# Kernel tuning notes

Hardware: AMD Instinct MI355X
Metric: run time of the kernel (lower is better)

The kernel has to match this reference:

```python
import jax, jax.numpy as jnp
import numpy as np

N = 100000
E = 1600000
H = 4
C = 128
F_IN = 182
D = H * C  # 512
NEG_SLOPE = 0.2
LN_EPS = 1e-5


def _p(key, shape, scale=0.05):
    return jax.random.normal(key, shape, dtype=jnp.float32) * scale


def setup_inputs() -> dict:
    key = jax.random.key(0)
    ks = jax.random.split(key, 20)
    x = jax.random.normal(ks[0], (N, F_IN), dtype=jnp.float32)
    edge_index = jax.random.randint(ks[1], (2, E), 0, N, dtype=jnp.int64)
    inp = {
        "x": x,
        "edge_index": edge_index,
        # GAT layer 1
        "W1": _p(ks[2], (F_IN, D)),
        "a_src1": _p(ks[3], (H, C)),
        "a_dst1": _p(ks[4], (H, C)),
        "b1": _p(ks[5], (D,)),
        "g1": jnp.ones((D,), jnp.float32),
        "be1": jnp.zeros((D,), jnp.float32),
        # GAT layer 2
        "W2": _p(ks[6], (D, D)),
        "a_src2": _p(ks[7], (H, C)),
        "a_dst2": _p(ks[8], (H, C)),
        "b2": _p(ks[9], (D,)),
        "g2": jnp.ones((D,), jnp.float32),
        "be2": jnp.zeros((D,), jnp.float32),
        # classifier MLP
        "Wc1": _p(ks[10], (D, D)),
        "bc1": jnp.zeros((D,), jnp.float32),
        "Wc2": _p(ks[11], (D, 2)),
        "bc2": jnp.zeros((2,), jnp.float32),
    }
    return inp


def _gat_conv(x, src, dst, W, a_src, a_dst, b):
    # x: [N, Fin] -> h: [N, H, C]
    h = (x @ W).reshape(N, H, C)
    # per-node attention contributions: [N, H]
    s_src = jnp.sum(h * a_src, axis=-1)
    s_dst = jnp.sum(h * a_dst, axis=-1)
    # per-edge raw score: [E+N, H]
    e = jax.nn.leaky_relu(s_src[src] + s_dst[dst], NEG_SLOPE)
    # segment softmax over incoming edges of each dst node
    emax = jax.ops.segment_max(e, dst, num_segments=N)
    p = jnp.exp(e - emax[dst])
    denom = jax.ops.segment_sum(p, dst, num_segments=N)
    alpha = p / denom[dst]  # [E+N, H]
    # weighted aggregation of source features: [N, H, C]
    out = jax.ops.segment_sum(alpha[:, :, None] * h[src], dst, num_segments=N)
    return out.reshape(N, D) + b


def _layer_norm(x, g, b):
    mu = jnp.mean(x, axis=-1, keepdims=True)
    var = jnp.mean(jnp.square(x - mu), axis=-1, keepdims=True)
    return (x - mu) * jax.lax.rsqrt(var + LN_EPS) * g + b


def reference(x, edge_index, W1, a_src1, a_dst1, b1, g1, be1,
              W2, a_src2, a_dst2, b2, g2, be2, Wc1, bc1, Wc2, bc2):
    # add self-loops (PyG GATConv default)
    loops = jnp.arange(N, dtype=edge_index.dtype)
    src = jnp.concatenate([edge_index[0], loops])
    dst = jnp.concatenate([edge_index[1], loops])

    h1 = _gat_conv(x, src, dst, W1, a_src1, a_dst1, b1)
    h1 = jax.nn.elu(_layer_norm(h1, g1, be1))
    h2 = _gat_conv(h1, src, dst, W2, a_src2, a_dst2, b2)
    h2 = jax.nn.elu(_layer_norm(h2, g2, be2))
    # classifier (dropout is identity in eval)
    z = jax.nn.relu(h2 @ Wc1 + bc1)
    return z @ Wc2 + bc2
```

## Files before the change

### kernel.cpp

```cpp
#include <hip/hip_runtime.h>
#include <math.h>

static constexpr int N_NODES = 100000;
static constexpr int N_EDGES = 1600000;
static constexpr int E_TOT   = N_NODES + N_EDGES;
static constexpr int D   = 512;
static constexpr int FIN = 182;
static constexpr int K1P = 192;
static constexpr int M_PAD = 100096;
static constexpr float NEG_SLOPE = 0.2f;
static constexpr float LN_EPS = 1e-5f;

typedef __attribute__((ext_vector_type(8))) short short8;
typedef __attribute__((ext_vector_type(4))) float floatx4;

__device__ __forceinline__ unsigned short f2bf(float f) {
  unsigned int x = __builtin_bit_cast(unsigned int, f);
  x += 0x7fffu + ((x >> 16) & 1u);
  return (unsigned short)(x >> 16);
}
__device__ __forceinline__ void unpack2(unsigned int w, float& lo, float& hi) {
  lo = __builtin_bit_cast(float, w << 16);
  hi = __builtin_bit_cast(float, w & 0xffff0000u);
}

typedef __attribute__((address_space(1))) const void gv_t;
typedef __attribute__((address_space(3))) void lv_t;
__device__ __forceinline__ void gll16(const void* g, void* l) {
  __builtin_amdgcn_global_load_lds((gv_t*)g, (lv_t*)l, 16, 0, 0);
}

__global__ __launch_bounds__(256) void k_init(int* __restrict__ deg,
                                              int* __restrict__ counter,
                                              int* __restrict__ flag) {
  int i = blockIdx.x * 256 + threadIdx.x;
  if (i < N_NODES) deg[i] = 0;
  if (i == 0) { *counter = 0; *flag = 0; }
}

__global__ __launch_bounds__(256) void k_detect(const int* __restrict__ ei,
                                                int* __restrict__ flag) {
  bool nz = false;
#pragma unroll
  for (int r = 0; r < 8; ++r) {
    int i = threadIdx.x + r * 256;
    nz |= (ei[2 * i + 1] != 0);
  }
  __shared__ int sh[4];
  int wv = threadIdx.x >> 6;
  if ((threadIdx.x & 63) == 0) sh[wv] = 0;
  __syncthreads();
  if (__any(nz) && (threadIdx.x & 63) == 0) sh[wv] = 1;
  __syncthreads();
  if (threadIdx.x == 0) *flag = sh[0] | sh[1] | sh[2] | sh[3];
}

__device__ __forceinline__ int edge_src(const int* ei, int f, int i) {
  return f ? ei[i] : ei[2 * i];
}
__device__ __forceinline__ int edge_dst(const int* ei, int f, int i) {
  return f ? ei[N_EDGES + i] : ei[2 * (N_EDGES + i)];
}

__global__ __launch_bounds__(256) void k_count(const int* __restrict__ ei,
                                               const int* __restrict__ flag,
                                               int* __restrict__ deg) {
  int i = blockIdx.x * 256 + threadIdx.x;
  if (i >= E_TOT) return;
  int f = *flag;
  int d = (i < N_EDGES) ? edge_dst(ei, f, i) : (i - N_EDGES);
  atomicAdd(deg + d, 1);
}

__global__ __launch_bounds__(256) void k_alloc(const int* __restrict__ deg,
                                               int* __restrict__ off,
                                               int* __restrict__ pos,
                                               int* __restrict__ counter) {
  int i = blockIdx.x * 256 + threadIdx.x;
  if (i >= N_NODES) return;
  int r = atomicAdd(counter, deg[i]);
  off[i] = r;
  pos[i] = r;
}

__global__ __launch_bounds__(256) void k_fill(const int* __restrict__ ei,
                                              const int* __restrict__ flag,
                                              int* __restrict__ pos,
                                              int* __restrict__ csr_src) {
  int i = blockIdx.x * 256 + threadIdx.x;
  if (i >= E_TOT) return;
  int f = *flag;
  int s, d;
  if (i < N_EDGES) { s = edge_src(ei, f, i); d = edge_dst(ei, f, i); }
  else             { s = d = i - N_EDGES; }
  int slot = atomicAdd(pos + d, 1);
  csr_src[slot] = s;
}

__global__ __launch_bounds__(256) void k_cvt_x(const float* __restrict__ x,
                                               unsigned short* __restrict__ xb) {
  int i = blockIdx.x * 256 + threadIdx.x;
  if (i >= N_NODES * K1P) return;
  int row = i / K1P, col = i - row * K1P;
  float v = (col < FIN) ? x[(size_t)row * FIN + col] : 0.f;
  xb[i] = f2bf(v);
}

__global__ __launch_bounds__(256) void k_cvt_wt(const float* __restrict__ W,
                                                unsigned short* __restrict__ Wt,
                                                int K, int Kpad) {
  int i = blockIdx.x * 256 + threadIdx.x;
  if (i >= 512 * Kpad) return;
  int n = i / Kpad, k = i - n * Kpad;
  Wt[i] = f2bf(k < K ? W[(size_t)k * 512 + n] : 0.f);
}

__global__ __launch_bounds__(256) void k_out_init(const float* __restrict__ bc2,
                                                  float* __restrict__ out) {
  int i = blockIdx.x * 256 + threadIdx.x;
  if (i < N_NODES) {
    float2 v; v.x = bc2[0]; v.y = bc2[1];
    ((float2*)out)[i] = v;
  }
}

__global__ __launch_bounds__(256)
void gemm_mfma(const unsigned short* __restrict__ A,
               const unsigned short* __restrict__ Bt,
               unsigned short* __restrict__ C,
               int lda)
{
  __shared__ unsigned short As[128 * 32];
  __shared__ unsigned short Bs[128 * 32];
  const int t    = threadIdx.x;
  const int w    = t >> 6;
  const int lane = t & 63;
  const int r    = lane & 15;
  const int q    = lane >> 4;
  const int bm   = blockIdx.y * 128;
  const int bn   = blockIdx.x * 128;
  const int wm   = (w >> 1) * 64;
  const int wn   = (w & 1) * 64;

  const int ch0 = (w * 2 + 0) * 64 + lane;
  const int ch1 = (w * 2 + 1) * 64 + lane;
  const unsigned short* gA0 = A + (size_t)(bm + (ch0 >> 2)) * lda + (ch0 & 3) * 8;
  const unsigned short* gA1 = A + (size_t)(bm + (ch1 >> 2)) * lda + (ch1 & 3) * 8;
  const unsigned short* gB0 = Bt + (size_t)(bn + (ch0 >> 2)) * lda + (ch0 & 3) * 8;
  const unsigned short* gB1 = Bt + (size_t)(bn + (ch1 >> 2)) * lda + (ch1 & 3) * 8;
  unsigned short* lA0 = As + (w * 2 + 0) * 512;
  unsigned short* lA1 = As + (w * 2 + 1) * 512;
  unsigned short* lB0 = Bs + (w * 2 + 0) * 512;
  unsigned short* lB1 = Bs + (w * 2 + 1) * 512;

  floatx4 acc[4][4] = {};

  for (int k0 = 0; k0 < lda; k0 += 32) {
    gll16(gA0 + k0, lA0);
    gll16(gA1 + k0, lA1);
    gll16(gB0 + k0, lB0);
    gll16(gB1 + k0, lB1);
    __syncthreads();

    short8 af[4], bfr[4];
#pragma unroll
    for (int im = 0; im < 4; ++im)
      af[im] = *(const short8*)(As + (wm + im * 16 + r) * 32 + q * 8);
#pragma unroll
    for (int in = 0; in < 4; ++in)
      bfr[in] = *(const short8*)(Bs + (wn + in * 16 + r) * 32 + q * 8);
#pragma unroll
    for (int im = 0; im < 4; ++im)
#pragma unroll
      for (int in = 0; in < 4; ++in)
        acc[im][in] = __builtin_amdgcn_mfma_f32_16x16x32_bf16(
            af[im], bfr[in], acc[im][in], 0, 0, 0);
    __syncthreads();
  }

#pragma unroll
  for (int in = 0; in < 4; ++in) {
    const int col = bn + wn + in * 16 + r;
#pragma unroll
    for (int im = 0; im < 4; ++im) {
      const size_t rowbase = (size_t)(bm + wm + im * 16 + q * 4) * 512 + col;
#pragma unroll
      for (int rr = 0; rr < 4; ++rr)
        C[rowbase + (size_t)rr * 512] = f2bf(acc[im][in][rr]);
    }
  }
}

__global__ __launch_bounds__(256)
void gemm_cls(const unsigned short* __restrict__ A,
              const unsigned short* __restrict__ Bt,
              const float* __restrict__ bc1,
              const float* __restrict__ Wc2,
              float* __restrict__ out,
              int lda)
{
  __shared__ unsigned short As[128 * 32];
  __shared__ unsigned short Bs[128 * 32];
  const int t    = threadIdx.x;
  const int w    = t >> 6;
  const int lane = t & 63;
  const int r    = lane & 15;
  const int q    = lane >> 4;
  const int bm   = blockIdx.y * 128;
  const int bn   = blockIdx.x * 128;
  const int wm   = (w >> 1) * 64;
  const int wn   = (w & 1) * 64;

  const int ch0 = (w * 2 + 0) * 64 + lane;
  const int ch1 = (w * 2 + 1) * 64 + lane;
  const unsigned short* gA0 = A + (size_t)(bm + (ch0 >> 2)) * lda + (ch0 & 3) * 8;
  const unsigned short* gA1 = A + (size_t)(bm + (ch1 >> 2)) * lda + (ch1 & 3) * 8;
  const unsigned short* gB0 = Bt + (size_t)(bn + (ch0 >> 2)) * lda + (ch0 & 3) * 8;
  const unsigned short* gB1 = Bt + (size_t)(bn + (ch1 >> 2)) * lda + (ch1 & 3) * 8;
  unsigned short* lA0 = As + (w * 2 + 0) * 512;
  unsigned short* lA1 = As + (w * 2 + 1) * 512;
  unsigned short* lB0 = Bs + (w * 2 + 0) * 512;
  unsigned short* lB1 = Bs + (w * 2 + 1) * 512;

  floatx4 acc[4][4] = {};

  for (int k0 = 0; k0 < lda; k0 += 32) {
    gll16(gA0 + k0, lA0);
    gll16(gA1 + k0, lA1);
    gll16(gB0 + k0, lB0);
    gll16(gB1 + k0, lB1);
    __syncthreads();

    short8 af[4], bfr[4];
#pragma unroll
    for (int im = 0; im < 4; ++im)
      af[im] = *(const short8*)(As + (wm + im * 16 + r) * 32 + q * 8);
#pragma unroll
    for (int in = 0; in < 4; ++in)
      bfr[in] = *(const short8*)(Bs + (wn + in * 16 + r) * 32 + q * 8);
#pragma unroll
    for (int im = 0; im < 4; ++im)
#pragma unroll
      for (int in = 0; in < 4; ++in)
        acc[im][in] = __builtin_amdgcn_mfma_f32_16x16x32_bf16(
            af[im], bfr[in], acc[im][in], 0, 0, 0);
    __syncthreads();
  }

  float p0[16], p1[16];
#pragma unroll
  for (int k = 0; k < 16; ++k) { p0[k] = 0.f; p1[k] = 0.f; }

#pragma unroll
  for (int in = 0; in < 4; ++in) {
    const int col = bn + wn + in * 16 + r;
    const float bv = bc1[col];
    const float w0 = Wc2[col * 2 + 0];
    const float w1 = Wc2[col * 2 + 1];
#pragma unroll
    for (int im = 0; im < 4; ++im)
#pragma unroll
      for (int rr = 0; rr < 4; ++rr) {
        float z = fmaxf(acc[im][in][rr] + bv, 0.f);
        p0[im * 4 + rr] += z * w0;
        p1[im * 4 + rr] += z * w1;
      }
  }
#pragma unroll
  for (int o2 = 1; o2 < 16; o2 <<= 1) {
#pragma unroll
    for (int k = 0; k < 16; ++k) {
      p0[k] += __shfl_xor(p0[k], o2);
      p1[k] += __shfl_xor(p1[k], o2);
    }
  }
  if (r == 0) {
#pragma unroll
    for (int im = 0; im < 4; ++im)
#pragma unroll
      for (int rr = 0; rr < 4; ++rr) {
        int row = bm + wm + im * 16 + q * 4 + rr;
        if (row < N_NODES) {
          atomicAdd(out + (size_t)row * 2,     p0[im * 4 + rr]);
          atomicAdd(out + (size_t)row * 2 + 1, p1[im * 4 + rr]);
        }
      }
  }
}

__global__ __launch_bounds__(256) void k_sdots(const unsigned short* __restrict__ h,
                                               const float* __restrict__ a_src,
                                               const float* __restrict__ a_dst,
                                               float2* __restrict__ ssc,
                                               float* __restrict__ s_dst,
                                               unsigned char* __restrict__ h8) {
  int node = blockIdx.x * 4 + (threadIdx.x >> 6);
  int lane = threadIdx.x & 63;
  if (node >= N_NODES) return;
  uint4 w = ((const uint4*)(h + (size_t)node * D))[lane];
  float v[8];
  unpack2(w.x, v[0], v[1]); unpack2(w.y, v[2], v[3]);
  unpack2(w.z, v[4], v[5]); unpack2(w.w, v[6], v[7]);

  float am = 0.f;
#pragma unroll
  for (int k = 0; k < 8; ++k) am = fmaxf(am, fabsf(v[k]));
#pragma unroll
  for (int o = 1; o < 16; o <<= 1) am = fmaxf(am, __shfl_xor(am, o));
  am = fmaxf(am, 1e-20f);
  const float qsc = 127.f / am;
  int qv[8];
#pragma unroll
  for (int k = 0; k < 8; ++k) qv[k] = (int)rintf(v[k] * qsc) + 128;
  uint2 pk;
  pk.x = (qv[0] & 255) | ((qv[1] & 255) << 8) | ((qv[2] & 255) << 16) | ((qv[3] & 255) << 24);
  pk.y = (qv[4] & 255) | ((qv[5] & 255) << 8) | ((qv[6] & 255) << 16) | ((qv[7] & 255) << 24);
  ((uint2*)(h8 + (size_t)node * 512))[lane] = pk;

  const float4* as = (const float4*)a_src;
  const float4* ad = (const float4*)a_dst;
  float4 s0 = as[lane*2], s1 = as[lane*2+1];
  float4 d0 = ad[lane*2], d1 = ad[lane*2+1];
  float ps = v[0]*s0.x + v[1]*s0.y + v[2]*s0.z + v[3]*s0.w
           + v[4]*s1.x + v[5]*s1.y + v[6]*s1.z + v[7]*s1.w;
  float pd = v[0]*d0.x + v[1]*d0.y + v[2]*d0.z + v[3]*d0.w
           + v[4]*d1.x + v[5]*d1.y + v[6]*d1.z + v[7]*d1.w;
#pragma unroll
  for (int o = 1; o < 16; o <<= 1) {
    ps += __shfl_xor(ps, o);
    pd += __shfl_xor(pd, o);
  }
  if ((lane & 15) == 0) {
    int hh = lane >> 4;
    float2 sc; sc.x = ps; sc.y = am * (1.f / 127.f);
    ssc[node*4 + hh] = sc;
    s_dst[node*4 + hh] = pd;
  }
}

__global__ __launch_bounds__(256) void k_aggregate(const unsigned char* __restrict__ h8,
                                                   const float2* __restrict__ ssc,
                                                   const int* __restrict__ csr_src,
                                                   const int* __restrict__ off,
                                                   const int* __restrict__ deg,
                                                   const float* __restrict__ s_dst,
                                                   const float* __restrict__ bvec,
                                                   const float* __restrict__ gvec,
                                                   const float* __restrict__ bevec,
                                                   unsigned short* __restrict__ out) {
  int node = blockIdx.x * 4 + (threadIdx.x >> 6);
  int lane = threadIdx.x & 63;
  if (node >= N_NODES) return;
  const int o   = __builtin_amdgcn_readfirstlane(off[node]);
  const int cnt = __builtin_amdgcn_readfirstlane(deg[node]);
  const int head = lane >> 4;
  const float sdH = s_dst[(size_t)node * 4 + head];

  float acc[8] = {0.f,0.f,0.f,0.f,0.f,0.f,0.f,0.f};
  float sum = 0.f, sum_ps = 0.f;

  int s_cur = __builtin_amdgcn_readfirstlane(csr_src[o]);
  uint2 w_cur = ((const uint2*)(h8 + (size_t)s_cur * 512))[lane];
  float2 fc_cur = ssc[(size_t)s_cur * 4 + head];

  for (int j = 0; j < cnt; ++j) {
    int jn = (j + 1 < cnt) ? (j + 1) : j;
    int s_nxt = __builtin_amdgcn_readfirstlane(csr_src[o + jn]);
    uint2 w_nxt = ((const uint2*)(h8 + (size_t)s_nxt * 512))[lane];
    float2 fc_nxt = ssc[(size_t)s_nxt * 4 + head];

    float e = fc_cur.x + sdH;
    e = (e > 0.f) ? e : NEG_SLOPE * e;
    float p = __expf(e);
    sum += p;
    float ps = p * fc_cur.y;
    sum_ps += ps;
    unsigned int wx = w_cur.x, wy = w_cur.y;
    acc[0] += ps * (float)( wx        & 255u);
    acc[1] += ps * (float)((wx >>  8) & 255u);
    acc[2] += ps * (float)((wx >> 16) & 255u);
    acc[3] += ps * (float)( wx >> 24);
    acc[4] += ps * (float)( wy        & 255u);
    acc[5] += ps * (float)((wy >>  8) & 255u);
    acc[6] += ps * (float)((wy >> 16) & 255u);
    acc[7] += ps * (float)( wy >> 24);

    s_cur = s_nxt; w_cur = w_nxt; fc_cur = fc_nxt;
  }

  const float inv = 1.f / sum;
  const float4* bb = (const float4*)bvec;
  float4 b0 = bb[lane*2], b1 = bb[lane*2+1];
  float bl[8] = {b0.x,b0.y,b0.z,b0.w,b1.x,b1.y,b1.z,b1.w};
#pragma unroll
  for (int k = 0; k < 8; ++k)
    acc[k] = (acc[k] - 128.f * sum_ps) * inv + bl[k];

  float ps2 = 0.f, pq = 0.f;
#pragma unroll
  for (int k = 0; k < 8; ++k) { ps2 += acc[k]; pq += acc[k]*acc[k]; }
#pragma unroll
  for (int o2 = 1; o2 < 64; o2 <<= 1) {
    ps2 += __shfl_xor(ps2, o2);
    pq  += __shfl_xor(pq, o2);
  }
  float mu  = ps2 * (1.f/512.f);
  float var = pq * (1.f/512.f) - mu*mu;
  float rstd = rsqrtf(var + LN_EPS);

  const float4* gg = (const float4*)gvec;
  const float4* ee = (const float4*)bevec;
  float4 g0 = gg[lane*2], g1 = gg[lane*2+1];
  float4 e0 = ee[lane*2], e1 = ee[lane*2+1];
  float gs[8] = {g0.x,g0.y,g0.z,g0.w,g1.x,g1.y,g1.z,g1.w};
  float es[8] = {e0.x,e0.y,e0.z,e0.w,e1.x,e1.y,e1.z,e1.w};

  unsigned short us[8];
#pragma unroll
  for (int k = 0; k < 8; ++k) {
    float y = (acc[k] - mu) * rstd * gs[k] + es[k];
    y = (y > 0.f) ? y : expm1f(y);
    us[k] = f2bf(y);
  }
  uint4 w;
  w.x = (unsigned int)us[0] | ((unsigned int)us[1] << 16);
  w.y = (unsigned int)us[2] | ((unsigned int)us[3] << 16);
  w.z = (unsigned int)us[4] | ((unsigned int)us[5] << 16);
  w.w = (unsigned int)us[6] | ((unsigned int)us[7] << 16);
  ((uint4*)(out + (size_t)node * D))[lane] = w;
}

extern "C" void kernel_launch(void* const* d_in, const int* in_sizes, int n_in,
                              void* d_out, int out_size, void* d_ws, size_t ws_size,
                              hipStream_t stream) {
  const float* x      = (const float*)d_in[0];
  const int*   ei     = (const int*)  d_in[1];
  const float* W1     = (const float*)d_in[2];
  const float* a_src1 = (const float*)d_in[3];
  const float* a_dst1 = (const float*)d_in[4];
  const float* b1     = (const float*)d_in[5];
  const float* g1     = (const float*)d_in[6];
  const float* be1    = (const float*)d_in[7];
  const float* W2     = (const float*)d_in[8];
  const float* a_src2 = (const float*)d_in[9];
  const float* a_dst2 = (const float*)d_in[10];
  const float* b2     = (const float*)d_in[11];
  const float* g2     = (const float*)d_in[12];
  const float* be2    = (const float*)d_in[13];
  const float* Wc1    = (const float*)d_in[14];
  const float* bc1    = (const float*)d_in[15];
  const float* Wc2    = (const float*)d_in[16];
  const float* bc2    = (const float*)d_in[17];
  float* outp = (float*)d_out;

  char* p = (char*)d_ws;
  auto alloc = [&](size_t bytes) {
    char* r = p;
    p += (bytes + 255) & ~(size_t)255;
    return r;
  };
  unsigned short* hbuf = (unsigned short*)alloc((size_t)M_PAD * D * 2);
  unsigned short* obuf = (unsigned short*)alloc((size_t)M_PAD * D * 2);
  unsigned short* w1t  = (unsigned short*)alloc((size_t)512 * K1P * 2);
  unsigned short* w2t  = (unsigned short*)alloc((size_t)512 * 512 * 2);
  unsigned short* wc1t = (unsigned short*)alloc((size_t)512 * 512 * 2);
  int*   csr_src = (int*)  alloc((size_t)E_TOT * 4);
  int*   deg     = (int*)  alloc((size_t)N_NODES * 4);
  int*   off     = (int*)  alloc((size_t)N_NODES * 4);
  int*   pos     = (int*)  alloc((size_t)N_NODES * 4);
  int*   counter = (int*)  alloc(256);
  int*   flag    = (int*)  alloc(256);
  float2* ssc    = (float2*)alloc((size_t)N_NODES * 4 * 8);
  float* s_dst   = (float*)alloc((size_t)N_NODES * 4 * 4);
  unsigned char* h8 = (unsigned char*)alloc((size_t)M_PAD * 512);
  unsigned short* xb = obuf;

  const int EB = (E_TOT + 255) / 256;
  const int NB = (N_NODES + 255) / 256;
  const int NW = (N_NODES + 3) / 4;
  dim3 gg(4, M_PAD / 128);

  k_init  <<<NB, 256, 0, stream>>>(deg, counter, flag);
  k_detect<<<1, 256, 0, stream>>>(ei, flag);
  k_count <<<EB, 256, 0, stream>>>(ei, flag, deg);
  k_alloc <<<NB, 256, 0, stream>>>(deg, off, pos, counter);
  k_fill  <<<EB, 256, 0, stream>>>(ei, flag, pos, csr_src);

  k_cvt_x <<<(N_NODES * K1P + 255) / 256, 256, 0, stream>>>(x, xb);
  k_cvt_wt<<<(512 * K1P + 255) / 256, 256, 0, stream>>>(W1, w1t, FIN, K1P);
  k_cvt_wt<<<(512 * 512 + 255) / 256, 256, 0, stream>>>(W2, w2t, 512, 512);
  k_cvt_wt<<<(512 * 512 + 255) / 256, 256, 0, stream>>>(Wc1, wc1t, 512, 512);
  k_out_init<<<NB, 256, 0, stream>>>(bc2, outp);

  gemm_mfma  <<<gg, 256, 0, stream>>>(xb, w1t, hbuf, K1P);
  k_sdots    <<<NW, 256, 0, stream>>>(hbuf, a_src1, a_dst1, ssc, s_dst, h8);
  k_aggregate<<<NW, 256, 0, stream>>>(h8, ssc, csr_src, off, deg,
                                      s_dst, b1, g1, be1, obuf);

  gemm_mfma  <<<gg, 256, 0, stream>>>(obuf, w2t, hbuf, 512);
  k_sdots    <<<NW, 256, 0, stream>>>(hbuf, a_src2, a_dst2, ssc, s_dst, h8);
  k_aggregate<<<NW, 256, 0, stream>>>(h8, ssc, csr_src, off, deg,
                                      s_dst, b2, g2, be2, obuf);

  gemm_cls   <<<gg, 256, 0, stream>>>(obuf, wc1t, bc1, Wc2, outp, 512);
}
```

Before: 1.012 ms.

## Fuse attention dots and int8 quantization into GEMM epilogue, merge detect into init

The per-node attention score dot products, per-head absmax and int8 quantization now run in the MFMA GEMM epilogue, using cross-lane shuffles and LDS reductions. This removes the bf16 h buffer write, its re-read by the separate k_sdots kernel, and one launch per layer. The h8 layout changes to a column interleave that follows the MFMA lane mapping, so the aggregate kernel now loads bias, gamma and beta and writes its output with a matching permuted index pattern. The edge-format detection is folded into k_init's first block to drop one more launch.

```diff
diff --git a/kernel.cpp b/kernel.cpp
--- a/kernel.cpp
+++ b/kernel.cpp
@@ -30,29 +30,30 @@
   __builtin_amdgcn_global_load_lds((gv_t*)g, (lv_t*)l, 16, 0, 0);
 }
 
-__global__ __launch_bounds__(256) void k_init(int* __restrict__ deg,
+__global__ __launch_bounds__(256) void k_init(const int* __restrict__ ei,
+                                              int* __restrict__ deg,
                                               int* __restrict__ counter,
                                               int* __restrict__ flag) {
   int i = blockIdx.x * 256 + threadIdx.x;
   if (i < N_NODES) deg[i] = 0;
-  if (i == 0) { *counter = 0; *flag = 0; }
-}
-
-__global__ __launch_bounds__(256) void k_detect(const int* __restrict__ ei,
-                                                int* __restrict__ flag) {
-  bool nz = false;
-#pragma unroll
-  for (int r = 0; r < 8; ++r) {
-    int i = threadIdx.x + r * 256;
-    nz |= (ei[2 * i + 1] != 0);
-  }
-  __shared__ int sh[4];
-  int wv = threadIdx.x >> 6;
-  if ((threadIdx.x & 63) == 0) sh[wv] = 0;
-  __syncthreads();
-  if (__any(nz) && (threadIdx.x & 63) == 0) sh[wv] = 1;
-  __syncthreads();
-  if (threadIdx.x == 0) *flag = sh[0] | sh[1] | sh[2] | sh[3];
+  if (blockIdx.x == 0) {
+    bool nz = false;
+#pragma unroll
+    for (int rp = 0; rp < 8; ++rp) {
+      int j = threadIdx.x + rp * 256;
+      nz |= (ei[2 * j + 1] != 0);
+    }
+    __shared__ int sh[4];
+    int wv = threadIdx.x >> 6;
+    if ((threadIdx.x & 63) == 0) sh[wv] = 0;
+    __syncthreads();
+    if (__any(nz) && (threadIdx.x & 63) == 0) sh[wv] = 1;
+    __syncthreads();
+    if (threadIdx.x == 0) {
+      *flag = sh[0] | sh[1] | sh[2] | sh[3];
+      *counter = 0;
+    }
+  }
 }
 
 __device__ __forceinline__ int edge_src(const int* ei, int f, int i) {
@@ -125,10 +126,14 @@
 }
 
 __global__ __launch_bounds__(256)
-void gemm_mfma(const unsigned short* __restrict__ A,
-               const unsigned short* __restrict__ Bt,
-               unsigned short* __restrict__ C,
-               int lda)
+void gemm_fused(const unsigned short* __restrict__ A,
+                const unsigned short* __restrict__ Bt,
+                const float* __restrict__ a_src,
+                const float* __restrict__ a_dst,
+                float2* __restrict__ ssc,
+                float* __restrict__ s_dst,
+                unsigned char* __restrict__ h8,
+                int lda)
 {
   __shared__ unsigned short As[128 * 32];
   __shared__ unsigned short Bs[128 * 32];
@@ -178,15 +183,82 @@
     __syncthreads();
   }
 
+  float* sred = (float*)As;
+  float* qscl = (float*)Bs;
+
+  float asv[4], adv[4];
 #pragma unroll
   for (int in = 0; in < 4; ++in) {
-    const int col = bn + wn + in * 16 + r;
-#pragma unroll
-    for (int im = 0; im < 4; ++im) {
-      const size_t rowbase = (size_t)(bm + wm + im * 16 + q * 4) * 512 + col;
-#pragma unroll
-      for (int rr = 0; rr < 4; ++rr)
-        C[rowbase + (size_t)rr * 512] = f2bf(acc[im][in][rr]);
+    asv[in] = a_src[bn + wn + in * 16 + r];
+    adv[in] = a_dst[bn + wn + in * 16 + r];
+  }
+#pragma unroll
+  for (int im = 0; im < 4; ++im) {
+    float ps_[4], pd_[4], pm_[4];
+#pragma unroll
+    for (int rr = 0; rr < 4; ++rr) {
+      float s = 0.f, d = 0.f, m = 0.f;
+#pragma unroll
+      for (int in = 0; in < 4; ++in) {
+        float v = acc[im][in][rr];
+        s += v * asv[in];
+        d += v * adv[in];
+        m = fmaxf(m, fabsf(v));
+      }
+      ps_[rr] = s; pd_[rr] = d; pm_[rr] = m;
+    }
+#pragma unroll
+    for (int o2 = 1; o2 < 16; o2 <<= 1) {
+#pragma unroll
+      for (int rr = 0; rr < 4; ++rr) {
+        ps_[rr] += __shfl_xor(ps_[rr], o2);
+        pd_[rr] += __shfl_xor(pd_[rr], o2);
+        pm_[rr] = fmaxf(pm_[rr], __shfl_xor(pm_[rr], o2));
+      }
+    }
+    if (r == 0) {
+#pragma unroll
+      for (int rr = 0; rr < 4; ++rr) {
+        int r64 = im * 16 + q * 4 + rr;
+        sred[(w * 64 + r64) * 4 + 0] = ps_[rr];
+        sred[(w * 64 + r64) * 4 + 1] = pd_[rr];
+        sred[(w * 64 + r64) * 4 + 2] = pm_[rr];
+      }
+    }
+  }
+  __syncthreads();
+
+  if (t < 128) {
+    int hf = t >> 6;
+    int r64 = t & 63;
+    const float* pa = sred + ((hf * 2 + 0) * 64 + r64) * 4;
+    const float* pb = sred + ((hf * 2 + 1) * 64 + r64) * 4;
+    float s  = pa[0] + pb[0];
+    float dd = pa[1] + pb[1];
+    float am = fmaxf(fmaxf(pa[2], pb[2]), 1e-20f);
+    qscl[t] = 127.f / am;
+    int node = bm + t;
+    if (node < N_NODES) {
+      float2 sc; sc.x = s; sc.y = am * (1.f / 127.f);
+      ssc[(size_t)node * 4 + blockIdx.x] = sc;
+      s_dst[(size_t)node * 4 + blockIdx.x] = dd;
+    }
+  }
+  __syncthreads();
+
+#pragma unroll
+  for (int im = 0; im < 4; ++im) {
+#pragma unroll
+    for (int rr = 0; rr < 4; ++rr) {
+      int lr = wm + im * 16 + q * 4 + rr;
+      float qs = qscl[lr];
+      unsigned int pk = 0;
+#pragma unroll
+      for (int in = 0; in < 4; ++in) {
+        int qv = (int)rintf(acc[im][in][rr] * qs) + 128;
+        pk |= (unsigned int)(qv & 255) << (8 * in);
+      }
+      *(unsigned int*)(h8 + (size_t)(bm + lr) * 512 + bn + wn + 4 * r) = pk;
     }
   }
 }
@@ -288,56 +360,6 @@
   }
 }
 
-__global__ __launch_bounds__(256) void k_sdots(const unsigned short* __restrict__ h,
-                                               const float* __restrict__ a_src,
-                                               const float* __restrict__ a_dst,
-                                               float2* __restrict__ ssc,
-                                               float* __restrict__ s_dst,
-                                               unsigned char* __restrict__ h8) {
-  int node = blockIdx.x * 4 + (threadIdx.x >> 6);
-  int lane = threadIdx.x & 63;
-  if (node >= N_NODES) return;
-  uint4 w = ((const uint4*)(h + (size_t)node * D))[lane];
-  float v[8];
-  unpack2(w.x, v[0], v[1]); unpack2(w.y, v[2], v[3]);
-  unpack2(w.z, v[4], v[5]); unpack2(w.w, v[6], v[7]);
-
-  float am = 0.f;
-#pragma unroll
-  for (int k = 0; k < 8; ++k) am = fmaxf(am, fabsf(v[k]));
-#pragma unroll
-  for (int o = 1; o < 16; o <<= 1) am = fmaxf(am, __shfl_xor(am, o));
-  am = fmaxf(am, 1e-20f);
-  const float qsc = 127.f / am;
-  int qv[8];
-#pragma unroll
-  for (int k = 0; k < 8; ++k) qv[k] = (int)rintf(v[k] * qsc) + 128;
-  uint2 pk;
-  pk.x = (qv[0] & 255) | ((qv[1] & 255) << 8) | ((qv[2] & 255) << 16) | ((qv[3] & 255) << 24);
-  pk.y = (qv[4] & 255) | ((qv[5] & 255) << 8) | ((qv[6] & 255) << 16) | ((qv[7] & 255) << 24);
-  ((uint2*)(h8 + (size_t)node * 512))[lane] = pk;
-
-  const float4* as = (const float4*)a_src;
-  const float4* ad = (const float4*)a_dst;
-  float4 s0 = as[lane*2], s1 = as[lane*2+1];
-  float4 d0 = ad[lane*2], d1 = ad[lane*2+1];
-  float ps = v[0]*s0.x + v[1]*s0.y + v[2]*s0.z + v[3]*s0.w
-           + v[4]*s1.x + v[5]*s1.y + v[6]*s1.z + v[7]*s1.w;
-  float pd = v[0]*d0.x + v[1]*d0.y + v[2]*d0.z + v[3]*d0.w
-           + v[4]*d1.x + v[5]*d1.y + v[6]*d1.z + v[7]*d1.w;
-#pragma unroll
-  for (int o = 1; o < 16; o <<= 1) {
-    ps += __shfl_xor(ps, o);
-    pd += __shfl_xor(pd, o);
-  }
-  if ((lane & 15) == 0) {
-    int hh = lane >> 4;
-    float2 sc; sc.x = ps; sc.y = am * (1.f / 127.f);
-    ssc[node*4 + hh] = sc;
-    s_dst[node*4 + hh] = pd;
-  }
-}
-
 __global__ __launch_bounds__(256) void k_aggregate(const unsigned char* __restrict__ h8,
                                                    const float2* __restrict__ ssc,
                                                    const int* __restrict__ csr_src,
@@ -354,6 +376,8 @@
   const int o   = __builtin_amdgcn_readfirstlane(off[node]);
   const int cnt = __builtin_amdgcn_readfirstlane(deg[node]);
   const int head = lane >> 4;
+  const int li   = lane & 15;
+  const int cbase = head * 128 + ((li & 8) ? 64 : 0) + ((2 * li) & 15);
   const float sdH = s_dst[(size_t)node * 4 + head];
 
   float acc[8] = {0.f,0.f,0.f,0.f,0.f,0.f,0.f,0.f};
@@ -389,9 +413,12 @@
   }
 
   const float inv = 1.f / sum;
-  const float4* bb = (const float4*)bvec;
-  float4 b0 = bb[lane*2], b1 = bb[lane*2+1];
-  float bl[8] = {b0.x,b0.y,b0.z,b0.w,b1.x,b1.y,b1.z,b1.w};
+  float bl[8];
+#pragma unroll
+  for (int k = 0; k < 4; ++k) {
+    float2 v2 = *(const float2*)(bvec + cbase + 16 * k);
+    bl[k] = v2.x; bl[k + 4] = v2.y;
+  }
 #pragma unroll
   for (int k = 0; k < 8; ++k)
     acc[k] = (acc[k] - 128.f * sum_ps) * inv + bl[k];
@@ -408,12 +435,14 @@
   float var = pq * (1.f/512.f) - mu*mu;
   float rstd = rsqrtf(var + LN_EPS);
 
-  const float4* gg = (const float4*)gvec;
-  const float4* ee = (const float4*)bevec;
-  float4 g0 = gg[lane*2], g1 = gg[lane*2+1];
-  float4 e0 = ee[lane*2], e1 = ee[lane*2+1];
-  float gs[8] = {g0.x,g0.y,g0.z,g0.w,g1.x,g1.y,g1.z,g1.w};
-  float es[8] = {e0.x,e0.y,e0.z,e0.w,e1.x,e1.y,e1.z,e1.w};
+  float gs[8], es[8];
+#pragma unroll
+  for (int k = 0; k < 4; ++k) {
+    float2 g2 = *(const float2*)(gvec  + cbase + 16 * k);
+    float2 e2 = *(const float2*)(bevec + cbase + 16 * k);
+    gs[k] = g2.x; gs[k + 4] = g2.y;
+    es[k] = e2.x; es[k + 4] = e2.y;
+  }
 
   unsigned short us[8];
 #pragma unroll
@@ -422,12 +451,11 @@
     y = (y > 0.f) ? y : expm1f(y);
     us[k] = f2bf(y);
   }
-  uint4 w;
-  w.x = (unsigned int)us[0] | ((unsigned int)us[1] << 16);
-  w.y = (unsigned int)us[2] | ((unsigned int)us[3] << 16);
-  w.z = (unsigned int)us[4] | ((unsigned int)us[5] << 16);
-  w.w = (unsigned int)us[6] | ((unsigned int)us[7] << 16);
-  ((uint4*)(out + (size_t)node * D))[lane] = w;
+#pragma unroll
+  for (int k = 0; k < 4; ++k) {
+    unsigned int wv2 = (unsigned int)us[k] | ((unsigned int)us[k + 4] << 16);
+    *(unsigned int*)(out + (size_t)node * D + cbase + 16 * k) = wv2;
+  }
 }
 
 extern "C" void kernel_launch(void* const* d_in, const int* in_sizes, int n_in,
@@ -459,7 +487,6 @@
     p += (bytes + 255) & ~(size_t)255;
     return r;
   };
-  unsigned short* hbuf = (unsigned short*)alloc((size_t)M_PAD * D * 2);
   unsigned short* obuf = (unsigned short*)alloc((size_t)M_PAD * D * 2);
   unsigned short* w1t  = (unsigned short*)alloc((size_t)512 * K1P * 2);
   unsigned short* w2t  = (unsigned short*)alloc((size_t)512 * 512 * 2);
@@ -480,8 +507,7 @@
   const int NW = (N_NODES + 3) / 4;
   dim3 gg(4, M_PAD / 128);
 
-  k_init  <<<NB, 256, 0, stream>>>(deg, counter, flag);
-  k_detect<<<1, 256, 0, stream>>>(ei, flag);
+  k_init  <<<NB, 256, 0, stream>>>(ei, deg, counter, flag);
   k_count <<<EB, 256, 0, stream>>>(ei, flag, deg);
   k_alloc <<<NB, 256, 0, stream>>>(deg, off, pos, counter);
   k_fill  <<<EB, 256, 0, stream>>>(ei, flag, pos, csr_src);
@@ -492,13 +518,11 @@
   k_cvt_wt<<<(512 * 512 + 255) / 256, 256, 0, stream>>>(Wc1, wc1t, 512, 512);
   k_out_init<<<NB, 256, 0, stream>>>(bc2, outp);
 
-  gemm_mfma  <<<gg, 256, 0, stream>>>(xb, w1t, hbuf, K1P);
-  k_sdots    <<<NW, 256, 0, stream>>>(hbuf, a_src1, a_dst1, ssc, s_dst, h8);
+  gemm_fused <<<gg, 256, 0, stream>>>(xb, w1t, a_src1, a_dst1, ssc, s_dst, h8, K1P);
   k_aggregate<<<NW, 256, 0, stream>>>(h8, ssc, csr_src, off, deg,
                                       s_dst, b1, g1, be1, obuf);
 
-  gemm_mfma  <<<gg, 256, 0, stream>>>(obuf, w2t, hbuf, 512);
-  k_sdots    <<<NW, 256, 0, stream>>>(hbuf, a_src2, a_dst2, ssc, s_dst, h8);
+  gemm_fused <<<gg, 256, 0, stream>>>(obuf, w2t, a_src2, a_dst2, ssc, s_dst, h8, 512);
   k_aggregate<<<NW, 256, 0, stream>>>(h8, ssc, csr_src, off, deg,
                                       s_dst, b2, g2, be2, obuf);
 
```

Result: no change. 1.017 ms (+0.5%).
